# Kernel tuning notes

Measured on AMD Instinct MI355X. Metric: run time of the kernel, lower is better.

The kernel has to match this reference:

```python
import jax, jax.numpy as jnp
import numpy as np

GROUPS = 16
EPS = 1e-5


def _dcn_v2(x, offset, mask, weight):
    """Modulated deformable 3x3 conv, stride=1, pad=1, no bias.
    x: [B,C,H,W], offset: [B,18,H,W] (dy,dx interleaved per kernel point),
    mask: [B,9,H,W] (modulation scalars), weight: [O,C,3,3]."""
    B, C, H, W = x.shape
    O = weight.shape[0]
    K = 9
    # kernel-point displacements, row-major (kh, kw): k = kh*3 + kw
    ky = jnp.repeat(jnp.arange(3) - 1, 3).astype(x.dtype)   # [9]
    kx = jnp.tile(jnp.arange(3) - 1, 3).astype(x.dtype)      # [9]
    dy = offset[:, 0::2]  # [B,9,H,W]
    dx = offset[:, 1::2]  # [B,9,H,W]
    hh = jnp.arange(H, dtype=x.dtype)
    ww = jnp.arange(W, dtype=x.dtype)
    # sampling coordinates (stride=1, pad=1)
    ys = hh[None, None, :, None] + ky[None, :, None, None] + dy  # [B,9,H,W]
    xs = ww[None, None, None, :] + kx[None, :, None, None] + dx  # [B,9,H,W]

    y0 = jnp.floor(ys)
    x0 = jnp.floor(xs)
    wy1 = ys - y0
    wx1 = xs - x0
    y0i = y0.astype(jnp.int32)
    x0i = x0.astype(jnp.int32)

    flat = x.reshape(B, C, H * W)

    def gather(yi, xi, w):
        # yi, xi, w: [B,9,H,W]; zero-padding outside the image
        valid = (yi >= 0) & (yi < H) & (xi >= 0) & (xi < W)
        idx = jnp.clip(yi, 0, H - 1) * W + jnp.clip(xi, 0, W - 1)  # [B,9,H,W]
        g = jnp.take_along_axis(flat, idx.reshape(B, 1, K * H * W), axis=2)
        g = g.reshape(B, C, K, H, W)
        return g * (w * valid.astype(x.dtype))[:, None]  # [B,C,9,H,W]

    val = (gather(y0i,     x0i,     (1 - wy1) * (1 - wx1))
         + gather(y0i,     x0i + 1, (1 - wy1) * wx1)
         + gather(y0i + 1, x0i,     wy1 * (1 - wx1))
         + gather(y0i + 1, x0i + 1, wy1 * wx1))
    val = val * mask[:, None]  # modulation
    # implicit GEMM: [B,C,9,H,W] x [O,C,9] -> [B,O,H,W]
    return jnp.einsum('bckhw,ock->bohw', val, weight.reshape(O, C, K))


def _group_norm(x, gamma, beta):
    B, C, H, W = x.shape
    xg = x.reshape(B, GROUPS, C // GROUPS, H, W)
    mu = xg.mean(axis=(2, 3, 4), keepdims=True)
    var = xg.var(axis=(2, 3, 4), keepdims=True)
    xn = ((xg - mu) * jax.lax.rsqrt(var + EPS)).reshape(B, C, H, W)
    return xn * gamma[None, :, None, None] + beta[None, :, None, None]


def setup_inputs() -> dict:
    key = jax.random.key(0)
    k1, k2, k3, k4 = jax.random.split(key, 4)
    B, C, O, H, W = 8, 256, 256, 64, 64
    x = jax.random.normal(k1, (B, C, H, W), dtype=jnp.float32)
    offset = jax.random.normal(k2, (B, 18, H, W), dtype=jnp.float32)
    mask = jax.random.uniform(k3, (B, 9, H, W), dtype=jnp.float32)
    weight = jax.random.normal(k4, (O, C, 3, 3), dtype=jnp.float32) * (1.0 / np.sqrt(C * 9))
    gamma = jnp.ones((O,), dtype=jnp.float32)
    beta = jnp.zeros((O,), dtype=jnp.float32)
    return {"x": x, "offset": offset, "mask": mask, "weight": weight,
            "gamma": gamma, "beta": beta}


def reference(x, offset, mask, weight, gamma, beta):
    out = _dcn_v2(x, offset, mask, weight)
    return _group_norm(out, gamma, beta)
```

## Files before the change

### kernel.cpp

```cpp
#include <hip/hip_runtime.h>
#include <stdint.h>


#define B_ 8
#define C_ 256
#define O_ 256
#define H_ 64
#define W_ 64
#define HW_ 4096
#define KTOT 2304
#define GROUPS_ 16
#define EPS_ 1e-5f
#define NSTEP 36
#define VROW 72

typedef float  f32x4  __attribute__((ext_vector_type(4)));
typedef short  short8 __attribute__((ext_vector_type(8)));
typedef unsigned int   u32;
typedef unsigned short u16;

#define XT_BYTES (B_*HW_*C_*2)
#define WIMG_OFF  XT_BYTES
#define WIMG_BYTES (72*16*64*16)
#define STATS_OFF (WIMG_OFF + WIMG_BYTES)

__device__ __forceinline__ u32 bf16r(float f) {
    u32 u = __float_as_uint(f);
    return (u + 0x7fffu + ((u >> 16) & 1u)) >> 16;
}
__device__ __forceinline__ u32 pack_bf16x2(float lo, float hi) {
    return bf16r(lo) | (bf16r(hi) << 16);
}
__device__ __forceinline__ float bflo(u32 u) { return __uint_as_float(u << 16); }
__device__ __forceinline__ float bfhi(u32 u) { return __uint_as_float(u & 0xffff0000u); }

__global__ void k_prep(const float* __restrict__ x, u16* __restrict__ xt,
                       const float* __restrict__ w, u16* __restrict__ wimg) {
    __shared__ float tile[32][33];
    const int bid = blockIdx.x;
    const int tid = threadIdx.x;
    if (bid < 8192) {
        const int pt = bid & 127, ct = (bid >> 7) & 7, b = bid >> 10;
        const int tx = tid & 31, ty = tid >> 5;
        const int p = pt * 32 + tx;
#pragma unroll
        for (int i = 0; i < 4; ++i) {
            int c = ct * 32 + ty + i * 8;
            tile[ty + i * 8][tx] = x[(((size_t)b * C_ + c) << 12) + p];
        }
        __syncthreads();
        const int cp = tx & 15;
        const int ps = ty + (tx >> 4) * 8;
#pragma unroll
        for (int i = 0; i < 2; ++i) {
            const int pl = ps + i * 16;
            u32 v = pack_bf16x2(tile[2 * cp][pl], tile[2 * cp + 1][pl]);
            *(u32*)&xt[((((size_t)b << 12) + pt * 32 + pl) << 8) + ct * 32 + 2 * cp] = v;
        }
    } else {
        const int sub = bid - 8192;
        const int k  = sub >> 3;
        const int c0 = (sub & 7) * 32;
#pragma unroll
        for (int i = 0; i < 4; ++i) {
            const int item = tid + i * 256;
            const int lane = item & 63;
            const int frag = item >> 6;
            const int col = lane & 15, quad = lane >> 4;
            const int n = frag * 16 + col;
            const float* src = w + (size_t)n * KTOT + (size_t)(c0 + quad * 8) * 9 + k;
            u32 o[4];
#pragma unroll
            for (int j = 0; j < 4; ++j)
                o[j] = pack_bf16x2(src[(size_t)(2 * j) * 9], src[(size_t)(2 * j + 1) * 9]);
            *(uint4*)&wimg[((size_t)sub * 1024 + item) * 8] = *(uint4*)o;
        }
    }
}

__device__ __forceinline__ void issue_gather(const u16* __restrict__ xtb,
                                             const float* __restrict__ mwp,
                                             const int* __restrict__ mip,
                                             int c0, int gpos, int oct,
                                             uint4 g[8], f32x4& mw) {
    mw = *(const f32x4*)&mwp[gpos * 4];
    const int4 ix = *(const int4*)&mip[gpos * 4];
    const u16* cb = xtb + c0 + oct * 16;
    const u16* p0 = cb + ((size_t)ix.x << 8);
    const u16* p1 = cb + ((size_t)ix.y << 8);
    const u16* p2 = cb + ((size_t)ix.z << 8);
    const u16* p3 = cb + ((size_t)ix.w << 8);
    g[0] = *(const uint4*)p0; g[1] = *(const uint4*)(p0 + 8);
    g[2] = *(const uint4*)p1; g[3] = *(const uint4*)(p1 + 8);
    g[4] = *(const uint4*)p2; g[5] = *(const uint4*)(p2 + 8);
    g[6] = *(const uint4*)p3; g[7] = *(const uint4*)(p3 + 8);
}

__device__ __forceinline__ void interp_store(const uint4 g[8], f32x4 mw, u16* dst) {
    float s[16];
#pragma unroll
    for (int i = 0; i < 16; ++i) s[i] = 0.f;
    const float ww[4] = {mw.x, mw.y, mw.z, mw.w};
#pragma unroll
    for (int cr = 0; cr < 4; ++cr) {
        const float wg = ww[cr];
        const uint4 a = g[2 * cr], bq = g[2 * cr + 1];
        s[0] += wg * bflo(a.x);  s[1] += wg * bfhi(a.x);
        s[2] += wg * bflo(a.y);  s[3] += wg * bfhi(a.y);
        s[4] += wg * bflo(a.z);  s[5] += wg * bfhi(a.z);
        s[6] += wg * bflo(a.w);  s[7] += wg * bfhi(a.w);
        s[8]  += wg * bflo(bq.x); s[9]  += wg * bfhi(bq.x);
        s[10] += wg * bflo(bq.y); s[11] += wg * bfhi(bq.y);
        s[12] += wg * bflo(bq.z); s[13] += wg * bfhi(bq.z);
        s[14] += wg * bflo(bq.w); s[15] += wg * bfhi(bq.w);
    }
    uint4 pk0, pk1;
    pk0.x = pack_bf16x2(s[0], s[1]);   pk0.y = pack_bf16x2(s[2], s[3]);
    pk0.z = pack_bf16x2(s[4], s[5]);   pk0.w = pack_bf16x2(s[6], s[7]);
    pk1.x = pack_bf16x2(s[8], s[9]);   pk1.y = pack_bf16x2(s[10], s[11]);
    pk1.z = pack_bf16x2(s[12], s[13]); pk1.w = pack_bf16x2(s[14], s[15]);
    *(uint4*)dst = pk0;
    *(uint4*)(dst + 8) = pk1;
}

__device__ __forceinline__ void load_wfrags(const u16* __restrict__ wimg, int sub0,
                                            int wid, int lane, short8 bfp[8]) {
#pragma unroll
    for (int kc = 0; kc < 2; ++kc)
#pragma unroll
        for (int ni = 0; ni < 4; ++ni)
            bfp[kc * 4 + ni] = *(const short8*)
                &wimg[(((size_t)(sub0 + kc) * 16 + wid * 4 + ni) * 64 + lane) * 8];
}

__launch_bounds__(256, 2)
__global__ void k_dcn(const u16* __restrict__ xt, const u16* __restrict__ wimg,
                      const float* __restrict__ offp, const float* __restrict__ mskp,
                      float* __restrict__ out, float* __restrict__ stats) {
    __shared__ __align__(16) float meta_w[9 * 64 * 4];
    __shared__ __align__(16) int   meta_i[9 * 64 * 4];
    __shared__ __align__(16) u16   lds_v[2][64 * VROW];

    const int tid = threadIdx.x;
    const int gid = blockIdx.x;
    const int b   = gid & 7;
    const int m0  = (gid >> 3) * 64;
    const int lane = tid & 63, wid = tid >> 6;
    const int col = lane & 15, quad = lane >> 4;
    const int gpos = tid >> 2, oct = tid & 3;

    const u16* xtb = xt + ((size_t)b << 20);

    for (int it = tid; it < 576; it += 256) {
        const int pos = it & 63, k = it >> 6;
        const int pg = m0 + pos;
        const int hh = pg >> 6, wwi = pg & 63;
        const float dy = offp[((size_t)(b * 18 + 2 * k) << 12) + pg];
        const float dx = offp[((size_t)(b * 18 + 2 * k + 1) << 12) + pg];
        const float mv = mskp[((size_t)(b * 9 + k) << 12) + pg];
        const float ys = (float)(hh + (k / 3) - 1) + dy;
        const float xs = (float)(wwi + (k % 3) - 1) + dx;
        const float y0f = floorf(ys), x0f = floorf(xs);
        const int y0 = (int)y0f, x0 = (int)x0f;
        const float wy1 = ys - y0f, wx1 = xs - x0f;
        const float wy0 = 1.f - wy1, wx0 = 1.f - wx1;
        const int y1 = y0 + 1, x1 = x0 + 1;
        const float vy0 = (y0 >= 0 && y0 < H_) ? 1.f : 0.f;
        const float vy1 = (y1 >= 0 && y1 < H_) ? 1.f : 0.f;
        const float vx0 = (x0 >= 0 && x0 < W_) ? 1.f : 0.f;
        const float vx1 = (x1 >= 0 && x1 < W_) ? 1.f : 0.f;
        const int y0c = min(max(y0, 0), H_ - 1), y1c = min(max(y1, 0), H_ - 1);
        const int x0c = min(max(x0, 0), W_ - 1), x1c = min(max(x1, 0), W_ - 1);
        meta_w[it * 4 + 0] = mv * wy0 * wx0 * vy0 * vx0;
        meta_w[it * 4 + 1] = mv * wy0 * wx1 * vy0 * vx1;
        meta_w[it * 4 + 2] = mv * wy1 * wx0 * vy1 * vx0;
        meta_w[it * 4 + 3] = mv * wy1 * wx1 * vy1 * vx1;
        meta_i[it * 4 + 0] = y0c * W_ + x0c;
        meta_i[it * 4 + 1] = y0c * W_ + x1c;
        meta_i[it * 4 + 2] = y1c * W_ + x0c;
        meta_i[it * 4 + 3] = y1c * W_ + x1c;
    }
    __syncthreads();

    uint4 g[8]; f32x4 mw; short8 bfp[8];
    issue_gather(xtb, &meta_w[0], &meta_i[0], 0, gpos, oct, g, mw);
    load_wfrags(wimg, 0, wid, lane, bfp);
    interp_store(g, mw, &lds_v[0][gpos * VROW + oct * 16]);
    __syncthreads();

    f32x4 acc[4][4];
#pragma unroll
    for (int i = 0; i < 4; ++i)
#pragma unroll
        for (int j = 0; j < 4; ++j) acc[i][j] = (f32x4){0.f, 0.f, 0.f, 0.f};

#pragma unroll 2
    for (int s = 0; s < NSTEP; ++s) {
        const int p = s & 1;
        short8 bcur[8];
#pragma unroll
        for (int i = 0; i < 8; ++i) bcur[i] = bfp[i];

        const bool pf = (s + 1 < NSTEP);
        if (pf) {
            const int sn = s + 1;
            const int kn = sn >> 2, c0n = (sn & 3) * 64;
            issue_gather(xtb, &meta_w[kn * 256], &meta_i[kn * 256], c0n, gpos, oct, g, mw);
            load_wfrags(wimg, 2 * sn, wid, lane, bfp);
        }

#pragma unroll
        for (int kc = 0; kc < 2; ++kc) {
            short8 af[4];
#pragma unroll
            for (int mi = 0; mi < 4; ++mi)
                af[mi] = *(const short8*)
                    &lds_v[p][(mi * 16 + col) * VROW + kc * 32 + quad * 8];
#pragma unroll
            for (int mi = 0; mi < 4; ++mi)
#pragma unroll
                for (int ni = 0; ni < 4; ++ni)
                    acc[mi][ni] = __builtin_amdgcn_mfma_f32_16x16x32_bf16(
                        af[mi], bcur[kc * 4 + ni], acc[mi][ni], 0, 0, 0);
        }

        if (pf) interp_store(g, mw, &lds_v[1 - p][gpos * VROW + oct * 16]);
        __syncthreads();
    }

#pragma unroll
    for (int mi = 0; mi < 4; ++mi)
#pragma unroll
        for (int ni = 0; ni < 4; ++ni) {
            const int o  = wid * 64 + ni * 16 + col;
            const int pg = m0 + mi * 16 + quad * 4;
            *(f32x4*)(out + (((size_t)b * O_ + o) << 12) + pg) = acc[mi][ni];
        }

#pragma unroll
    for (int ni = 0; ni < 4; ++ni) {
        float s = 0.f, s2 = 0.f;
#pragma unroll
        for (int mi = 0; mi < 4; ++mi) {
            f32x4 v = acc[mi][ni];
            s  += v.x + v.y + v.z + v.w;
            s2 += v.x * v.x + v.y * v.y + v.z * v.z + v.w * v.w;
        }
#pragma unroll
        for (int d = 32; d > 0; d >>= 1) {
            s  += __shfl_xor(s, d, 64);
            s2 += __shfl_xor(s2, d, 64);
        }
        if (lane == 0) {
            const int gI = wid * 4 + ni;
            atomicAdd(&stats[b * GROUPS_ + gI], s);
            atomicAdd(&stats[128 + b * GROUPS_ + gI], s2);
        }
    }
}

__global__ void k_gn(float* __restrict__ out, const float* __restrict__ stats,
                     const float* __restrict__ gamma, const float* __restrict__ beta) {
    const int blk = blockIdx.x;
    const int b = blk >> 8, o = blk & 255;
    const int gI = b * GROUPS_ + (o >> 4);
    const float n = 65536.f;
    const float mean = stats[gI] / n;
    const float var  = stats[128 + gI] / n - mean * mean;
    const float inv  = rsqrtf(fmaxf(var, 0.f) + EPS_);
    const float scale = inv * gamma[o];
    const float shift = beta[o] - mean * scale;
    f32x4* p = (f32x4*)(out + ((size_t)blk << 12));
    const int t = threadIdx.x;
#pragma unroll
    for (int i = 0; i < 4; ++i) {
        f32x4 v = p[t + i * 256];
        p[t + i * 256] = v * scale + shift;
    }
}

extern "C" void kernel_launch(void* const* d_in, const int* in_sizes, int n_in,
                              void* d_out, int out_size, void* d_ws, size_t ws_size,
                              hipStream_t stream) {
    const float* x     = (const float*)d_in[0];
    const float* offp  = (const float*)d_in[1];
    const float* mskp  = (const float*)d_in[2];
    const float* w     = (const float*)d_in[3];
    const float* gamma = (const float*)d_in[4];
    const float* beta  = (const float*)d_in[5];
    float* outp = (float*)d_out;

    u16*   xt    = (u16*)d_ws;
    u16*   wimg  = (u16*)((char*)d_ws + WIMG_OFF);
    float* stats = (float*)((char*)d_ws + STATS_OFF);

    hipMemsetAsync(stats, 0, 1024, stream);
    k_prep<<<dim3(8192 + 72), dim3(256), 0, stream>>>(x, xt, w, wimg);
    k_dcn<<<dim3(512), dim3(256), 0, stream>>>(xt, wimg, offp, mskp, outp, stats);
    k_gn<<<dim3(2048), dim3(256), 0, stream>>>(outp, stats, gamma, beta);
}
```

Before: 201.3 us.

## Halve DCN block tile to 32 positions and deepen gather pipeline

```diff
diff --git a/kernel.cpp b/kernel.cpp
--- a/kernel.cpp
+++ b/kernel.cpp
@@ -11,8 +11,8 @@
 #define KTOT 2304
 #define GROUPS_ 16
 #define EPS_ 1e-5f
-#define NSTEP 36
-#define VROW 72
+#define NSTEP 72
+#define VROW 40
 
 typedef float  f32x4  __attribute__((ext_vector_type(4)));
 typedef short  short8 __attribute__((ext_vector_type(8)));
@@ -33,6 +33,10 @@
 }
 __device__ __forceinline__ float bflo(u32 u) { return __uint_as_float(u << 16); }
 __device__ __forceinline__ float bfhi(u32 u) { return __uint_as_float(u & 0xffff0000u); }
+
+__device__ __forceinline__ void barrier_lds() {
+    asm volatile("s_waitcnt lgkmcnt(0)\n\ts_barrier" ::: "memory");
+}
 
 __global__ void k_prep(const float* __restrict__ x, u16* __restrict__ xt,
                        const float* __restrict__ w, u16* __restrict__ wimg) {
@@ -78,81 +82,55 @@
     }
 }
 
-__device__ __forceinline__ void issue_gather(const u16* __restrict__ xtb,
+__device__ __forceinline__ void issue_gather(const u16* __restrict__ cb,
                                              const float* __restrict__ mwp,
                                              const int* __restrict__ mip,
-                                             int c0, int gpos, int oct,
-                                             uint4 g[8], f32x4& mw) {
+                                             int gpos, uint2 g[4], f32x4& mw) {
     mw = *(const f32x4*)&mwp[gpos * 4];
     const int4 ix = *(const int4*)&mip[gpos * 4];
-    const u16* cb = xtb + c0 + oct * 16;
-    const u16* p0 = cb + ((size_t)ix.x << 8);
-    const u16* p1 = cb + ((size_t)ix.y << 8);
-    const u16* p2 = cb + ((size_t)ix.z << 8);
-    const u16* p3 = cb + ((size_t)ix.w << 8);
-    g[0] = *(const uint4*)p0; g[1] = *(const uint4*)(p0 + 8);
-    g[2] = *(const uint4*)p1; g[3] = *(const uint4*)(p1 + 8);
-    g[4] = *(const uint4*)p2; g[5] = *(const uint4*)(p2 + 8);
-    g[6] = *(const uint4*)p3; g[7] = *(const uint4*)(p3 + 8);
-}
-
-__device__ __forceinline__ void interp_store(const uint4 g[8], f32x4 mw, u16* dst) {
-    float s[16];
-#pragma unroll
-    for (int i = 0; i < 16; ++i) s[i] = 0.f;
+    g[0] = *(const uint2*)(cb + ix.x);
+    g[1] = *(const uint2*)(cb + ix.y);
+    g[2] = *(const uint2*)(cb + ix.z);
+    g[3] = *(const uint2*)(cb + ix.w);
+}
+
+__device__ __forceinline__ void interp_store(const uint2 g[4], f32x4 mw, u16* dst) {
+    f32x4 a = (f32x4){0.f, 0.f, 0.f, 0.f};
     const float ww[4] = {mw.x, mw.y, mw.z, mw.w};
 #pragma unroll
     for (int cr = 0; cr < 4; ++cr) {
         const float wg = ww[cr];
-        const uint4 a = g[2 * cr], bq = g[2 * cr + 1];
-        s[0] += wg * bflo(a.x);  s[1] += wg * bfhi(a.x);
-        s[2] += wg * bflo(a.y);  s[3] += wg * bfhi(a.y);
-        s[4] += wg * bflo(a.z);  s[5] += wg * bfhi(a.z);
-        s[6] += wg * bflo(a.w);  s[7] += wg * bfhi(a.w);
-        s[8]  += wg * bflo(bq.x); s[9]  += wg * bfhi(bq.x);
-        s[10] += wg * bflo(bq.y); s[11] += wg * bfhi(bq.y);
-        s[12] += wg * bflo(bq.z); s[13] += wg * bfhi(bq.z);
-        s[14] += wg * bflo(bq.w); s[15] += wg * bfhi(bq.w);
-    }
-    uint4 pk0, pk1;
-    pk0.x = pack_bf16x2(s[0], s[1]);   pk0.y = pack_bf16x2(s[2], s[3]);
-    pk0.z = pack_bf16x2(s[4], s[5]);   pk0.w = pack_bf16x2(s[6], s[7]);
-    pk1.x = pack_bf16x2(s[8], s[9]);   pk1.y = pack_bf16x2(s[10], s[11]);
-    pk1.z = pack_bf16x2(s[12], s[13]); pk1.w = pack_bf16x2(s[14], s[15]);
-    *(uint4*)dst = pk0;
-    *(uint4*)(dst + 8) = pk1;
-}
-
-__device__ __forceinline__ void load_wfrags(const u16* __restrict__ wimg, int sub0,
-                                            int wid, int lane, short8 bfp[8]) {
-#pragma unroll
-    for (int kc = 0; kc < 2; ++kc)
-#pragma unroll
-        for (int ni = 0; ni < 4; ++ni)
-            bfp[kc * 4 + ni] = *(const short8*)
-                &wimg[(((size_t)(sub0 + kc) * 16 + wid * 4 + ni) * 64 + lane) * 8];
-}
-
-__launch_bounds__(256, 2)
+        a.x += wg * bflo(g[cr].x);
+        a.y += wg * bfhi(g[cr].x);
+        a.z += wg * bflo(g[cr].y);
+        a.w += wg * bfhi(g[cr].y);
+    }
+    uint2 pk;
+    pk.x = pack_bf16x2(a.x, a.y);
+    pk.y = pack_bf16x2(a.z, a.w);
+    *(uint2*)dst = pk;
+}
+
+__launch_bounds__(256, 4)
 __global__ void k_dcn(const u16* __restrict__ xt, const u16* __restrict__ wimg,
                       const float* __restrict__ offp, const float* __restrict__ mskp,
                       float* __restrict__ out, float* __restrict__ stats) {
-    __shared__ __align__(16) float meta_w[9 * 64 * 4];
-    __shared__ __align__(16) int   meta_i[9 * 64 * 4];
-    __shared__ __align__(16) u16   lds_v[2][64 * VROW];
+    __shared__ __align__(16) float meta_w[9 * 32 * 4];
+    __shared__ __align__(16) int   meta_i[9 * 32 * 4];
+    __shared__ __align__(16) u16   lds_v[2][32 * VROW];
 
     const int tid = threadIdx.x;
     const int gid = blockIdx.x;
     const int b   = gid & 7;
-    const int m0  = (gid >> 3) * 64;
+    const int m0  = (gid >> 3) * 32;
     const int lane = tid & 63, wid = tid >> 6;
     const int col = lane & 15, quad = lane >> 4;
-    const int gpos = tid >> 2, oct = tid & 3;
+    const int gpos = tid >> 3, oct = tid & 7;
 
     const u16* xtb = xt + ((size_t)b << 20);
 
-    for (int it = tid; it < 576; it += 256) {
-        const int pos = it & 63, k = it >> 6;
+    for (int it = tid; it < 288; it += 256) {
+        const int pos = it & 31, k = it >> 5;
         const int pg = m0 + pos;
         const int hh = pg >> 6, wwi = pg & 63;
         const float dy = offp[((size_t)(b * 18 + 2 * k) << 12) + pg];
@@ -175,61 +153,62 @@
         meta_w[it * 4 + 1] = mv * wy0 * wx1 * vy0 * vx1;
         meta_w[it * 4 + 2] = mv * wy1 * wx0 * vy1 * vx0;
         meta_w[it * 4 + 3] = mv * wy1 * wx1 * vy1 * vx1;
-        meta_i[it * 4 + 0] = y0c * W_ + x0c;
-        meta_i[it * 4 + 1] = y0c * W_ + x1c;
-        meta_i[it * 4 + 2] = y1c * W_ + x0c;
-        meta_i[it * 4 + 3] = y1c * W_ + x1c;
+        meta_i[it * 4 + 0] = (y0c * W_ + x0c) << 8;
+        meta_i[it * 4 + 1] = (y0c * W_ + x1c) << 8;
+        meta_i[it * 4 + 2] = (y1c * W_ + x0c) << 8;
+        meta_i[it * 4 + 3] = (y1c * W_ + x1c) << 8;
     }
     __syncthreads();
 
-    uint4 g[8]; f32x4 mw; short8 bfp[8];
-    issue_gather(xtb, &meta_w[0], &meta_i[0], 0, gpos, oct, g, mw);
-    load_wfrags(wimg, 0, wid, lane, bfp);
-    interp_store(g, mw, &lds_v[0][gpos * VROW + oct * 16]);
+    uint2 gg[2][4]; f32x4 mwr[2];
+    issue_gather(xtb + 0 + oct * 4, &meta_w[0], &meta_i[0], gpos, gg[0], mwr[0]);
+    interp_store(gg[0], mwr[0], &lds_v[0][gpos * VROW + oct * 4]);
+    issue_gather(xtb + 32 + oct * 4, &meta_w[0], &meta_i[0], gpos, gg[1], mwr[1]);
     __syncthreads();
 
-    f32x4 acc[4][4];
-#pragma unroll
-    for (int i = 0; i < 4; ++i)
+    f32x4 acc[2][4];
+#pragma unroll
+    for (int i = 0; i < 2; ++i)
 #pragma unroll
         for (int j = 0; j < 4; ++j) acc[i][j] = (f32x4){0.f, 0.f, 0.f, 0.f};
 
 #pragma unroll 2
     for (int s = 0; s < NSTEP; ++s) {
-        const int p = s & 1;
-        short8 bcur[8];
-#pragma unroll
-        for (int i = 0; i < 8; ++i) bcur[i] = bfp[i];
-
-        const bool pf = (s + 1 < NSTEP);
-        if (pf) {
-            const int sn = s + 1;
-            const int kn = sn >> 2, c0n = (sn & 3) * 64;
-            issue_gather(xtb, &meta_w[kn * 256], &meta_i[kn * 256], c0n, gpos, oct, g, mw);
-            load_wfrags(wimg, 2 * sn, wid, lane, bfp);
-        }
-
-#pragma unroll
-        for (int kc = 0; kc < 2; ++kc) {
-            short8 af[4];
-#pragma unroll
-            for (int mi = 0; mi < 4; ++mi)
-                af[mi] = *(const short8*)
-                    &lds_v[p][(mi * 16 + col) * VROW + kc * 32 + quad * 8];
-#pragma unroll
-            for (int mi = 0; mi < 4; ++mi)
-#pragma unroll
-                for (int ni = 0; ni < 4; ++ni)
-                    acc[mi][ni] = __builtin_amdgcn_mfma_f32_16x16x32_bf16(
-                        af[mi], bcur[kc * 4 + ni], acc[mi][ni], 0, 0, 0);
-        }
-
-        if (pf) interp_store(g, mw, &lds_v[1 - p][gpos * VROW + oct * 16]);
-        __syncthreads();
-    }
-
-#pragma unroll
-    for (int mi = 0; mi < 4; ++mi)
+        const int pa = s & 1;
+
+        short8 bcur[4];
+#pragma unroll
+        for (int ni = 0; ni < 4; ++ni)
+            bcur[ni] = *(const short8*)
+                &wimg[(((size_t)s * 16 + wid * 4 + ni) * 64 + lane) * 8];
+
+        if (s + 2 < NSTEP) {
+            const int sn = s + 2;
+            const int kn = sn >> 3, c0n = (sn & 7) * 32;
+            issue_gather(xtb + c0n + oct * 4, &meta_w[kn * 128], &meta_i[kn * 128],
+                         gpos, gg[pa], mwr[pa]);
+        }
+
+        short8 af[2];
+#pragma unroll
+        for (int mi = 0; mi < 2; ++mi)
+            af[mi] = *(const short8*)&lds_v[pa][(mi * 16 + col) * VROW + quad * 8];
+
+#pragma unroll
+        for (int mi = 0; mi < 2; ++mi)
+#pragma unroll
+            for (int ni = 0; ni < 4; ++ni)
+                acc[mi][ni] = __builtin_amdgcn_mfma_f32_16x16x32_bf16(
+                    af[mi], bcur[ni], acc[mi][ni], 0, 0, 0);
+
+        if (s + 1 < NSTEP)
+            interp_store(gg[1 - pa], mwr[1 - pa], &lds_v[1 - pa][gpos * VROW + oct * 4]);
+
+        barrier_lds();
+    }
+
+#pragma unroll
+    for (int mi = 0; mi < 2; ++mi)
 #pragma unroll
         for (int ni = 0; ni < 4; ++ni) {
             const int o  = wid * 64 + ni * 16 + col;
@@ -241,7 +220,7 @@
     for (int ni = 0; ni < 4; ++ni) {
         float s = 0.f, s2 = 0.f;
 #pragma unroll
-        for (int mi = 0; mi < 4; ++mi) {
+        for (int mi = 0; mi < 2; ++mi) {
             f32x4 v = acc[mi][ni];
             s  += v.x + v.y + v.z + v.w;
             s2 += v.x * v.x + v.y * v.y + v.z * v.z + v.w * v.w;
@@ -296,6 +275,6 @@
 
     hipMemsetAsync(stats, 0, 1024, stream);
     k_prep<<<dim3(8192 + 72), dim3(256), 0, stream>>>(x, xt, w, wimg);
-    k_dcn<<<dim3(512), dim3(256), 0, stream>>>(xt, wimg, offp, mskp, outp, stats);
+    k_dcn<<<dim3(1024), dim3(256), 0, stream>>>(xt, wimg, offp, mskp, outp, stats);
     k_gn<<<dim3(2048), dim3(256), 0, stream>>>(outp, stats, gamma, beta);
 }
```

After: 229.7 us. 14.1% more time.
